# Kernel optimization log

Measured on AMD Instinct MI355X. Metric: run time of the kernel, lower is better.

Reference implementation:

```python
import jax, jax.numpy as jnp
import numpy as np

B, T, N, D = 128, 5, 64, 4
F1, F2 = 32, 32            # cnn filters
H = 128                    # mlp hidden units
PRED_STEPS = 8

# fully-connected adjacency without self-loops (fc_matrix)
_adj = np.ones((N, N)) - np.eye(N)
SRC, TGT = np.where(_adj)
SRC = jnp.asarray(SRC)
TGT = jnp.asarray(TGT)
E = int(SRC.shape[0])      # N*(N-1) = 4032


def _glorot(key, shape):
    fan_in = shape[-2] if len(shape) >= 2 else shape[0]
    return jax.random.normal(key, shape, jnp.float32) * float(1.0 / np.sqrt(fan_in))


def setup_inputs() -> dict:
    key = jax.random.key(0)
    ks = jax.random.split(key, 16)
    inp = {
        'time_segs': jax.random.normal(ks[0], (B, T, N, D), jnp.float32),
        # Conv1D over time: two valid convs, kernel 3
        'cw1': _glorot(ks[1], (3, D, F1)), 'cb1': jnp.zeros((F1,), jnp.float32),
        'cw2': _glorot(ks[2], (3, F1, F2)), 'cb2': jnp.zeros((F2,), jnp.float32),
        # edge encoder MLP: 2*F2 -> H -> H
        'ew1': _glorot(ks[3], (2 * F2, H)), 'eb1': jnp.zeros((H,), jnp.float32),
        'ew2': _glorot(ks[4], (H, H)), 'eb2': jnp.zeros((H,), jnp.float32),
        # node encoder MLP: H -> H -> H
        'nw1': _glorot(ks[5], (H, H)), 'nb1': jnp.zeros((H,), jnp.float32),
        'nw2': _glorot(ks[6], (H, H)), 'nb2': jnp.zeros((H,), jnp.float32),
        # node decoder MLP: (D + H) -> H -> H
        'dw1': _glorot(ks[7], (D + H, H)), 'db1': jnp.zeros((H,), jnp.float32),
        'dw2': _glorot(ks[8], (H, H)), 'db2': jnp.zeros((H,), jnp.float32),
        # output dense: H -> D
        'ow': _glorot(ks[9], (H, D)), 'ob': jnp.zeros((D,), jnp.float32),
    }
    return inp


def _mlp(x, w1, b1, w2, b2):
    h = jax.nn.relu(x @ w1 + b1)
    return jax.nn.relu(h @ w2 + b2)


def _conv_time(x, w, b):
    # x: [B, N, t, C]; valid conv (kernel 3) over time axis, relu
    b_, n_, t_, c_ = x.shape
    y = jax.lax.conv_general_dilated(
        x.reshape(b_ * n_, t_, c_), w, window_strides=(1,), padding='VALID',
        dimension_numbers=('NWC', 'WIO', 'NWC'))
    y = jax.nn.relu(y + b)
    return y.reshape(b_, n_, y.shape[1], y.shape[2])


def reference(time_segs, cw1, cb1, cw2, cb2, ew1, eb1, ew2, eb2,
              nw1, nb1, nw2, nb2, dw1, db1, dw2, db2, ow, ob):
    # [B, T, N, D] -> [B, N, T, D]
    window = jnp.transpose(time_segs, (0, 2, 1, 3))
    preds = []
    for _ in range(PRED_STEPS):
        # condense time: [B, N, 5, D] -> [B, N, 1, F2]
        h = _conv_time(window, cw1, cb1)
        h = _conv_time(h, cw2, cb2)
        # gather source/target node states per edge -> [B, E, 1, 2*F2]
        edge_in = jnp.concatenate([h[:, SRC], h[:, TGT]], axis=-1)
        edge_msg = _mlp(edge_in, ew1, eb1, ew2, eb2)           # [B, E, 1, H]
        # scatter-sum edge messages to target nodes -> [B, N, 1, H]
        node_msg = jnp.zeros((window.shape[0], N, 1, edge_msg.shape[-1]),
                             edge_msg.dtype).at[:, TGT].add(edge_msg)
        node_msg = _mlp(node_msg, nw1, nb1, nw2, nb2)
        prev = window[:, :, -1:, :]                            # [B, N, 1, D]
        dec = _mlp(jnp.concatenate([prev, node_msg], axis=-1), dw1, db1, dw2, db2)
        nxt = dec @ ow + ob + prev                             # residual, [B, N, 1, D]
        preds.append(nxt)
        window = jnp.concatenate([window[:, :, 1:, :], nxt], axis=2)
    out = jnp.concatenate(preds, axis=2)                       # [B, N, P, D]
    return jnp.transpose(out, (0, 2, 1, 3))                    # [B, P, N, D]
```

## Files before the change

kernel.cpp:

```cpp
#include <hip/hip_runtime.h>

#define WROW 52
#define TG 8

typedef _Float16 half_t;
typedef _Float16 half8 __attribute__((ext_vector_type(8)));
typedef float f32x4 __attribute__((ext_vector_type(4)));

#define SC 0.0009765625f

__device__ __forceinline__ unsigned pkrtz(float a, float b) {
  auto v = __builtin_amdgcn_cvt_pkrtz(a, b);
  return *(unsigned*)&v;
}

template<int LANES>
__device__ __forceinline__ void conv_proj(
    int lane, int gid, float* cp,
    const float* __restrict__ cw1, const float* __restrict__ cb1,
    const float* __restrict__ cw2, const float* __restrict__ cb2,
    const float* __restrict__ ew1,
    float* __restrict__ an, float* __restrict__ bn)
{
  #pragma unroll
  for (int o = 0; o < 96 / LANES; ++o) {
    int idx = lane + o * LANES;
    int tt = idx >> 5, f = idx & 31;
    float a = cb1[f];
    #pragma unroll
    for (int kt = 0; kt < 3; ++kt)
      #pragma unroll
      for (int d = 0; d < 4; ++d)
        a = fmaf(cp[(tt + kt) * 4 + d], cw1[(kt * 4 + d) * 32 + f], a);
    cp[32 + idx] = fmaxf(a, 0.f);
  }
  __syncthreads();
  #pragma unroll
  for (int o = 0; o < 32 / LANES; ++o) {
    int f = lane + o * LANES;
    float a = cb2[f];
    #pragma unroll
    for (int kt = 0; kt < 3; ++kt)
      for (int f1 = 0; f1 < 32; ++f1)
        a = fmaf(cp[32 + kt * 32 + f1], cw2[(kt * 32 + f1) * 32 + f], a);
    cp[128 + f] = fmaxf(a, 0.f);
  }
  __syncthreads();
  #pragma unroll
  for (int o = 0; o < 128 / LANES; ++o) {
    int j = lane + o * LANES;
    float a = 0.f, bb = 0.f;
    for (int f = 0; f < 32; ++f) {
      float h = cp[128 + f];
      a  = fmaf(h, ew1[f * 128 + j], a);
      bb = fmaf(h, ew1[(32 + f) * 128 + j], bb);
    }
    an[gid * 128 + j] = a * SC;
    bn[gid * 128 + j] = bb * SC;
  }
}

__global__ __launch_bounds__(256) void k_init(
    const float* __restrict__ ts,
    const float* __restrict__ cw1, const float* __restrict__ cb1,
    const float* __restrict__ cw2, const float* __restrict__ cb2,
    const float* __restrict__ ew1,
    float* __restrict__ win, float* __restrict__ an, float* __restrict__ bn)
{
  __shared__ float cp[16 * 160];
  int blk = blockIdx.x;
  int b = blk >> 2, n0 = (blk & 3) << 4;
  int tid = threadIdx.x;
  int ln = tid >> 4, lane = tid & 15;
  int n = n0 + ln;
  int gid = b * 64 + n;
  float* mycp = cp + ln * 160;
  for (int idx = lane; idx < 20; idx += 16) {
    int tt = idx >> 2, d = idx & 3;
    float v = ts[((b * 5 + tt) * 64 + n) * 4 + d];
    mycp[idx] = v;
    win[gid * WROW + idx] = v;
  }
  __syncthreads();
  conv_proj<16>(lane, gid, mycp, cw1, cb1, cw2, cb2, ew1, an, bn);
}

__global__ __launch_bounds__(256) void k_wsplit(
    const float* __restrict__ ew2, const float* __restrict__ nw1,
    const float* __restrict__ nw2, const float* __restrict__ dw1,
    const float* __restrict__ dw2, half_t* __restrict__ dst)
{
  int mat = blockIdx.x >> 6;
  const float* src = (mat == 0) ? ew2 : (mat == 1) ? nw1 : (mat == 2) ? nw2
                   : (mat == 3) ? (dw1 + 512) : dw2;
  half_t* dh = dst + mat * 2 * 16384;
  half_t* dl = dh + 16384;
  int g = (blockIdx.x & 63) * 256 + threadIdx.x;
  int k = g >> 7, col = g & 127;
  float x = src[g];
  _Float16 hi = (_Float16)x;
  float lo = x - (float)hi;
  int c = col >> 4, kb = k >> 5, kk = k & 31;
  int lane = ((kk >> 3) << 4) | (col & 15);
  int j = kk & 7;
  int idx = ((c * 4 + kb) * 64 + lane) * 8 + j;
  dh[idx] = hi;
  dl[idx] = (_Float16)lo;
}

__global__ __launch_bounds__(256, 2) void k_edge_v8(
    const float* __restrict__ an, const float* __restrict__ bn,
    const float* __restrict__ eb1, const float* __restrict__ eb2,
    const half_t* __restrict__ Bh, const half_t* __restrict__ Bl,
    float* __restrict__ nm)
{
  __shared__ __align__(16) half_t sAh[8192];
  __shared__ __align__(16) half_t sAl[8192];
  __shared__ float s_bt[TG * 128];
  int blk = blockIdx.x;
  int b = blk & 127, t0 = (blk >> 7) * TG;
  int tid = threadIdx.x;
  int w = tid >> 6, lane = tid & 63;

  #pragma unroll
  for (int i = 0; i < TG * 128 / 256; ++i) {
    int idx = tid + (i << 8);
    int tt = idx >> 7, j = idx & 127;
    s_bt[idx] = bn[((b << 6) + t0 + tt) * 128 + j] + eb1[j] * SC;
  }

  float au[4][8];
  {
    int kb8 = tid >> 4, sl = tid & 15;
    #pragma unroll
    for (int it = 0; it < 4; ++it) {
      const float* ap = an + (b << 13) + ((it * 16 + sl) << 7) + (kb8 << 3);
      float4 x0 = *(const float4*)ap;
      float4 x1 = *(const float4*)(ap + 4);
      au[it][0] = x0.x; au[it][1] = x0.y; au[it][2] = x0.z; au[it][3] = x0.w;
      au[it][4] = x1.x; au[it][5] = x1.y; au[it][6] = x1.z; au[it][7] = x1.w;
    }
  }

  half8 rbh[2][4], rbl[2][4];
  #pragma unroll
  for (int cc = 0; cc < 2; ++cc)
    #pragma unroll
    for (int kb = 0; kb < 4; ++kb) {
      int c = w * 2 + cc;
      rbh[cc][kb] = *(const half8*)(Bh + ((c * 4 + kb) * 64 + lane) * 8);
      rbl[cc][kb] = *(const half8*)(Bl + ((c * 4 + kb) * 64 + lane) * 8);
    }

  float bias0 = eb2[(w * 2 + 0) * 16 + (lane & 15)];
  float bias1 = eb2[(w * 2 + 1) * 16 + (lane & 15)];
  int rowoff = (lane >> 4) * 4;

  __syncthreads();

  for (int tt = 0; tt < TG; ++tt) {
    {
      const float* bp = s_bt + (tt << 7) + ((tid >> 4) << 3);
      float4 b0 = *(const float4*)bp;
      float4 b1 = *(const float4*)(bp + 4);
      float bs[8] = {b0.x, b0.y, b0.z, b0.w, b1.x, b1.y, b1.z, b1.w};
      #pragma unroll
      for (int it = 0; it < 4; ++it) {
        int u = tid + (it << 8);
        float h32[8], l32[8];
        #pragma unroll
        for (int i = 0; i < 8; ++i) {
          float x = fmaxf(au[it][i] + bs[i], 0.f);
          float h = __uint_as_float(__float_as_uint(x) & 0xffffe000u);
          h32[i] = h;
          l32[i] = x - h;
        }
        unsigned hw[4], lw[4];
        #pragma unroll
        for (int p = 0; p < 4; ++p) {
          hw[p] = pkrtz(h32[2 * p], h32[2 * p + 1]);
          lw[p] = pkrtz(l32[2 * p], l32[2 * p + 1]);
        }
        *(uint4*)(sAh + u * 8) = make_uint4(hw[0], hw[1], hw[2], hw[3]);
        *(uint4*)(sAl + u * 8) = make_uint4(lw[0], lw[1], lw[2], lw[3]);
      }
    }
    __syncthreads();

    f32x4 acc[4][2];
    #pragma unroll
    for (int rr = 0; rr < 4; ++rr)
      #pragma unroll
      for (int cc = 0; cc < 2; ++cc)
        acc[rr][cc] = (f32x4){0.f, 0.f, 0.f, 0.f};

    #pragma unroll
    for (int kb = 0; kb < 4; ++kb) {
      half8 ah[4], al[4];
      #pragma unroll
      for (int rr = 0; rr < 4; ++rr) {
        ah[rr] = *(const half8*)(sAh + ((rr * 4 + kb) * 64 + lane) * 8);
        al[rr] = *(const half8*)(sAl + ((rr * 4 + kb) * 64 + lane) * 8);
      }
      #pragma unroll
      for (int cc = 0; cc < 2; ++cc)
        #pragma unroll
        for (int rr = 0; rr < 4; ++rr) {
          acc[rr][cc] = __builtin_amdgcn_mfma_f32_16x16x32_f16(ah[rr], rbh[cc][kb], acc[rr][cc], 0, 0, 0);
          acc[rr][cc] = __builtin_amdgcn_mfma_f32_16x16x32_f16(ah[rr], rbl[cc][kb], acc[rr][cc], 0, 0, 0);
          acc[rr][cc] = __builtin_amdgcn_mfma_f32_16x16x32_f16(al[rr], rbh[cc][kb], acc[rr][cc], 0, 0, 0);
        }
    }

    int t = t0 + tt;
    float csum0 = 0.f, csum1 = 0.f;
    #pragma unroll
    for (int rr = 0; rr < 4; ++rr) {
      int sbase = rr * 16 + rowoff;
      #pragma unroll
      for (int q = 0; q < 4; ++q) {
        int s = sbase + q;
        float y0 = acc[rr][0][q] * 1024.f + bias0;
        float y1 = acc[rr][1][q] * 1024.f + bias1;
        if (s != t) {
          csum0 += fmaxf(y0, 0.f);
          csum1 += fmaxf(y1, 0.f);
        }
      }
    }
    csum0 += __shfl_xor(csum0, 16, 64);
    csum0 += __shfl_xor(csum0, 32, 64);
    csum1 += __shfl_xor(csum1, 16, 64);
    csum1 += __shfl_xor(csum1, 32, 64);
    if (lane < 32)
      nm[((b << 6) + t) * 128 + w * 32 + lane] = (lane < 16) ? csum0 : csum1;
    __syncthreads();
  }
}

__global__ __launch_bounds__(256) void k_nd_mfma(
    int step,
    const float* __restrict__ nm,
    const half_t* __restrict__ wsp,
    const float* __restrict__ nb1, const float* __restrict__ nb2,
    const float* __restrict__ dw1, const float* __restrict__ db1,
    const float* __restrict__ db2,
    const float* __restrict__ ow,  const float* __restrict__ ob,
    const float* __restrict__ cw1, const float* __restrict__ cb1,
    const float* __restrict__ cw2, const float* __restrict__ cb2,
    const float* __restrict__ ew1,
    float* __restrict__ win, float* __restrict__ an, float* __restrict__ bn,
    float* __restrict__ out)
{
  __shared__ __align__(16) float Xraw[16][132];
  __shared__ __align__(16) half_t sAh[2048];
  __shared__ __align__(16) half_t sAl[2048];
  __shared__ float sP[16][4];
  __shared__ float s_dw1a[4 * 128];
  __shared__ float s_nxt[16][4];
  __shared__ float cp[16 * 160];

  int blk = blockIdx.x;
  int b = blk >> 2, n0 = (blk & 3) << 4;
  int tid = threadIdx.x;
  int w = tid >> 6, lane = tid & 63;

  #pragma unroll
  for (int i = 0; i < 2; ++i) {
    int idx = tid + (i << 8);
    int row = idx >> 5, jf = idx & 31;
    *(float4*)&Xraw[row][jf << 2] =
        *(const float4*)(nm + ((b * 64 + n0 + row) << 7) + (jf << 2));
  }
  if (tid < 64) {
    int ln = tid >> 2, d = tid & 3;
    sP[ln][d] = win[(b * 64 + n0 + ln) * WROW + (step + 4) * 4 + d];
  }
  for (int idx = tid; idx < 512; idx += 256) s_dw1a[idx] = dw1[idx];
  __syncthreads();

  auto splitX = [&]() {
    int kb = tid >> 6, l = tid & 63;
    int row = l & 15, k0 = (kb << 5) + ((l >> 4) << 3);
    float h32[8], l32[8];
    #pragma unroll
    for (int i = 0; i < 8; ++i) {
      float x = Xraw[row][k0 + i] * SC;
      float h = __uint_as_float(__float_as_uint(x) & 0xffffe000u);
      h32[i] = h;
      l32[i] = x - h;
    }
    unsigned hw[4], lw[4];
    #pragma unroll
    for (int p = 0; p < 4; ++p) {
      hw[p] = pkrtz(h32[2 * p], h32[2 * p + 1]);
      lw[p] = pkrtz(l32[2 * p], l32[2 * p + 1]);
    }
    *(uint4*)(sAh + tid * 8) = make_uint4(hw[0], hw[1], hw[2], hw[3]);
    *(uint4*)(sAl + tid * 8) = make_uint4(lw[0], lw[1], lw[2], lw[3]);
  };

  auto layerM = [&](const half_t* Wh, const half_t* Wl,
                    const float* bias, bool withP) {
    splitX();
    __syncthreads();
    #pragma unroll
    for (int cc = 0; cc < 2; ++cc) {
      int c = w * 2 + cc;
      int col = c * 16 + (lane & 15);
      int row0 = (lane >> 4) * 4;
      float bj = bias[col];
      f32x4 acc;
      #pragma unroll
      for (int q = 0; q < 4; ++q) {
        float v = bj;
        if (withP) {
          #pragma unroll
          for (int d = 0; d < 4; ++d)
            v = fmaf(sP[row0 + q][d], s_dw1a[d * 128 + col], v);
        }
        acc[q] = v * SC;
      }
      #pragma unroll
      for (int kb = 0; kb < 4; ++kb) {
        half8 ah = *(const half8*)(sAh + ((kb << 6) + lane) * 8);
        half8 al = *(const half8*)(sAl + ((kb << 6) + lane) * 8);
        half8 bh = *(const half8*)(Wh + ((c * 4 + kb) * 64 + lane) * 8);
        half8 bl = *(const half8*)(Wl + ((c * 4 + kb) * 64 + lane) * 8);
        acc = __builtin_amdgcn_mfma_f32_16x16x32_f16(ah, bh, acc, 0, 0, 0);
        acc = __builtin_amdgcn_mfma_f32_16x16x32_f16(ah, bl, acc, 0, 0, 0);
        acc = __builtin_amdgcn_mfma_f32_16x16x32_f16(al, bh, acc, 0, 0, 0);
      }
      #pragma unroll
      for (int q = 0; q < 4; ++q)
        Xraw[row0 + q][col] = fmaxf(acc[q] * 1024.f, 0.f);
    }
    __syncthreads();
  };

  const half_t* nh1 = wsp + 2 * 16384;  const half_t* nl1 = nh1 + 16384;
  const half_t* nh2 = wsp + 4 * 16384;  const half_t* nl2 = nh2 + 16384;
  const half_t* dh1 = wsp + 6 * 16384;  const half_t* dl1 = dh1 + 16384;
  const half_t* dh2 = wsp + 8 * 16384;  const half_t* dl2 = dh2 + 16384;

  layerM(nh1, nl1, nb1, false);
  layerM(nh2, nl2, nb2, false);
  layerM(dh1, dl1, db1, true);
  layerM(dh2, dl2, db2, false);

  {
    int ln = tid >> 4, d = (tid >> 2) & 3, kq = tid & 3;
    float cs = 0.f;
    #pragma unroll
    for (int i = 0; i < 32; ++i) {
      int k = (kq << 5) + i;
      cs = fmaf(Xraw[ln][k], ow[k * 4 + d], cs);
    }
    cs += __shfl_xor(cs, 1, 64);
    cs += __shfl_xor(cs, 2, 64);
    if ((tid & 3) == 0) {
      float a = cs + ob[d] + sP[ln][d];
      int n = n0 + ln, gid = b * 64 + n;
      win[gid * WROW + (step + 5) * 4 + d] = a;
      out[((b * 8 + step) * 64 + n) * 4 + d] = a;
      s_nxt[ln][d] = a;
    }
  }
  __syncthreads();

  if (step < 7) {
    int ln = tid >> 4, lane2 = tid & 15;
    int gid = b * 64 + n0 + ln;
    float* mycp = cp + ln * 160;
    mycp[lane2] = win[gid * WROW + (step + 1) * 4 + lane2];
    if (lane2 < 4) mycp[16 + lane2] = s_nxt[ln][lane2];
    __syncthreads();
    conv_proj<16>(lane2, gid, mycp, cw1, cb1, cw2, cb2, ew1, an, bn);
  }
}

extern "C" void kernel_launch(void* const* d_in, const int* in_sizes, int n_in,
                              void* d_out, int out_size, void* d_ws, size_t ws_size,
                              hipStream_t stream) {
  (void)in_sizes; (void)n_in; (void)out_size; (void)ws_size;
  const float* ts  = (const float*)d_in[0];
  const float* cw1 = (const float*)d_in[1];
  const float* cb1 = (const float*)d_in[2];
  const float* cw2 = (const float*)d_in[3];
  const float* cb2 = (const float*)d_in[4];
  const float* ew1 = (const float*)d_in[5];
  const float* eb1 = (const float*)d_in[6];
  const float* ew2 = (const float*)d_in[7];
  const float* eb2 = (const float*)d_in[8];
  const float* nw1 = (const float*)d_in[9];
  const float* nb1 = (const float*)d_in[10];
  const float* nw2 = (const float*)d_in[11];
  const float* nb2 = (const float*)d_in[12];
  const float* dw1 = (const float*)d_in[13];
  const float* db1 = (const float*)d_in[14];
  const float* dw2 = (const float*)d_in[15];
  const float* db2 = (const float*)d_in[16];
  const float* ow  = (const float*)d_in[17];
  const float* ob  = (const float*)d_in[18];
  float* out = (float*)d_out;
  float* ws  = (float*)d_ws;
  float* win = ws;
  float* an  = win + 425984;
  float* bn  = an + 1048576;
  float* nmb = bn + 1048576;
  half_t* wsp = (half_t*)(nmb + 1048576);
  half_t* Bh = wsp;
  half_t* Bl = Bh + 16384;

  hipLaunchKernelGGL(k_wsplit, dim3(320), dim3(256), 0, stream,
                     ew2, nw1, nw2, dw1, dw2, wsp);
  hipLaunchKernelGGL(k_init, dim3(512), dim3(256), 0, stream,
                     ts, cw1, cb1, cw2, cb2, ew1, win, an, bn);
  for (int k = 0; k < 8; ++k) {
    hipLaunchKernelGGL(k_edge_v8, dim3(1024), dim3(256), 0, stream,
                       an, bn, eb1, eb2, Bh, Bl, nmb);
    hipLaunchKernelGGL(k_nd_mfma, dim3(512), dim3(256), 0, stream,
                       k, nmb, wsp, nb1, nb2, dw1, db1, db2,
                       ow, ob, cw1, cb1, cw2, cb2, ew1, win, an, bn, out);
  }
}
```

Before: 610.4 us.

## Fuse edge and node/decoder kernels into one per-step kernel with ping-pong buffers

Merges the edge-message kernel and the node/decoder kernel into a single kernel per prediction step. Each block now handles 16 target nodes (TG raised to 16), keeps the summed node messages in shared memory, and runs the node and decoder MLPs and the next-step conv projection directly. This removes the global round-trip of the node-message buffer and halves the number of launches. The an/bn projections are double-buffered because blocks now write the next step's projections while other blocks may still be reading the current ones. The cost is fewer, heavier blocks (512 instead of 1024) and a shared-memory union that has to stay alias-safe.

After: 531.2 us. -13.0%, faster.

```diff
diff --git a/kernel.cpp b/kernel.cpp
--- a/kernel.cpp
+++ b/kernel.cpp
@@ -1,7 +1,7 @@
 #include <hip/hip_runtime.h>
 
 #define WROW 52
-#define TG 8
+#define TG 16
 
 typedef _Float16 half_t;
 typedef _Float16 half8 __attribute__((ext_vector_type(8)));
@@ -108,25 +108,46 @@
   dl[idx] = (_Float16)lo;
 }
 
-__global__ __launch_bounds__(256, 2) void k_edge_v8(
-    const float* __restrict__ an, const float* __restrict__ bn,
+__global__ __launch_bounds__(256, 2) void k_step(
+    int step,
+    const float* __restrict__ anR, const float* __restrict__ bnR,
+    float* __restrict__ anW, float* __restrict__ bnW,
     const float* __restrict__ eb1, const float* __restrict__ eb2,
-    const half_t* __restrict__ Bh, const half_t* __restrict__ Bl,
-    float* __restrict__ nm)
+    const half_t* __restrict__ wsp,
+    const float* __restrict__ nb1, const float* __restrict__ nb2,
+    const float* __restrict__ dw1, const float* __restrict__ db1,
+    const float* __restrict__ db2,
+    const float* __restrict__ ow,  const float* __restrict__ ob,
+    const float* __restrict__ cw1, const float* __restrict__ cb1,
+    const float* __restrict__ cw2, const float* __restrict__ cb2,
+    const float* __restrict__ ew1,
+    float* __restrict__ win, float* __restrict__ out)
 {
-  __shared__ __align__(16) half_t sAh[8192];
-  __shared__ __align__(16) half_t sAl[8192];
-  __shared__ float s_bt[TG * 128];
+  __shared__ __align__(16) unsigned char smem[40960];
+  __shared__ __align__(16) float X[16][132];
+  half_t* sAh = (half_t*)smem;
+  half_t* sAl = (half_t*)(smem + 16384);
+  float*  s_bt = (float*)(smem + 32768);
+  half_t* nAh = (half_t*)smem;
+  half_t* nAl = (half_t*)(smem + 4096);
+  float*  cp     = (float*)(smem + 16640);
+  float*  s_dw1a = (float*)(smem + 26880);
+  float (*sP)[4]   = (float(*)[4])(smem + 28928);
+  float (*s_nxt)[4] = (float(*)[4])(smem + 29184);
+
   int blk = blockIdx.x;
   int b = blk & 127, t0 = (blk >> 7) * TG;
   int tid = threadIdx.x;
   int w = tid >> 6, lane = tid & 63;
 
+  const half_t* Bh = wsp;
+  const half_t* Bl = wsp + 16384;
+
   #pragma unroll
   for (int i = 0; i < TG * 128 / 256; ++i) {
     int idx = tid + (i << 8);
     int tt = idx >> 7, j = idx & 127;
-    s_bt[idx] = bn[((b << 6) + t0 + tt) * 128 + j] + eb1[j] * SC;
+    s_bt[idx] = bnR[((b << 6) + t0 + tt) * 128 + j] + eb1[j] * SC;
   }
 
   float au[4][8];
@@ -134,7 +155,7 @@
     int kb8 = tid >> 4, sl = tid & 15;
     #pragma unroll
     for (int it = 0; it < 4; ++it) {
-      const float* ap = an + (b << 13) + ((it * 16 + sl) << 7) + (kb8 << 3);
+      const float* ap = anR + (b << 13) + ((it * 16 + sl) << 7) + (kb8 << 3);
       float4 x0 = *(const float4*)ap;
       float4 x1 = *(const float4*)(ap + 4);
       au[it][0] = x0.x; au[it][1] = x0.y; au[it][2] = x0.z; au[it][3] = x0.w;
@@ -233,48 +254,13 @@
     csum1 += __shfl_xor(csum1, 16, 64);
     csum1 += __shfl_xor(csum1, 32, 64);
     if (lane < 32)
-      nm[((b << 6) + t) * 128 + w * 32 + lane] = (lane < 16) ? csum0 : csum1;
+      X[tt][w * 32 + lane] = (lane < 16) ? csum0 : csum1;
     __syncthreads();
   }
-}
-
-__global__ __launch_bounds__(256) void k_nd_mfma(
-    int step,
-    const float* __restrict__ nm,
-    const half_t* __restrict__ wsp,
-    const float* __restrict__ nb1, const float* __restrict__ nb2,
-    const float* __restrict__ dw1, const float* __restrict__ db1,
-    const float* __restrict__ db2,
-    const float* __restrict__ ow,  const float* __restrict__ ob,
-    const float* __restrict__ cw1, const float* __restrict__ cb1,
-    const float* __restrict__ cw2, const float* __restrict__ cb2,
-    const float* __restrict__ ew1,
-    float* __restrict__ win, float* __restrict__ an, float* __restrict__ bn,
-    float* __restrict__ out)
-{
-  __shared__ __align__(16) float Xraw[16][132];
-  __shared__ __align__(16) half_t sAh[2048];
-  __shared__ __align__(16) half_t sAl[2048];
-  __shared__ float sP[16][4];
-  __shared__ float s_dw1a[4 * 128];
-  __shared__ float s_nxt[16][4];
-  __shared__ float cp[16 * 160];
-
-  int blk = blockIdx.x;
-  int b = blk >> 2, n0 = (blk & 3) << 4;
-  int tid = threadIdx.x;
-  int w = tid >> 6, lane = tid & 63;
-
-  #pragma unroll
-  for (int i = 0; i < 2; ++i) {
-    int idx = tid + (i << 8);
-    int row = idx >> 5, jf = idx & 31;
-    *(float4*)&Xraw[row][jf << 2] =
-        *(const float4*)(nm + ((b * 64 + n0 + row) << 7) + (jf << 2));
-  }
+
   if (tid < 64) {
     int ln = tid >> 2, d = tid & 3;
-    sP[ln][d] = win[(b * 64 + n0 + ln) * WROW + (step + 4) * 4 + d];
+    sP[ln][d] = win[(b * 64 + t0 + ln) * WROW + (step + 4) * 4 + d];
   }
   for (int idx = tid; idx < 512; idx += 256) s_dw1a[idx] = dw1[idx];
   __syncthreads();
@@ -285,7 +271,7 @@
     float h32[8], l32[8];
     #pragma unroll
     for (int i = 0; i < 8; ++i) {
-      float x = Xraw[row][k0 + i] * SC;
+      float x = X[row][k0 + i] * SC;
       float h = __uint_as_float(__float_as_uint(x) & 0xffffe000u);
       h32[i] = h;
       l32[i] = x - h;
@@ -296,8 +282,8 @@
       hw[p] = pkrtz(h32[2 * p], h32[2 * p + 1]);
       lw[p] = pkrtz(l32[2 * p], l32[2 * p + 1]);
     }
-    *(uint4*)(sAh + tid * 8) = make_uint4(hw[0], hw[1], hw[2], hw[3]);
-    *(uint4*)(sAl + tid * 8) = make_uint4(lw[0], lw[1], lw[2], lw[3]);
+    *(uint4*)(nAh + tid * 8) = make_uint4(hw[0], hw[1], hw[2], hw[3]);
+    *(uint4*)(nAl + tid * 8) = make_uint4(lw[0], lw[1], lw[2], lw[3]);
   };
 
   auto layerM = [&](const half_t* Wh, const half_t* Wl,
@@ -323,8 +309,8 @@
       }
       #pragma unroll
       for (int kb = 0; kb < 4; ++kb) {
-        half8 ah = *(const half8*)(sAh + ((kb << 6) + lane) * 8);
-        half8 al = *(const half8*)(sAl + ((kb << 6) + lane) * 8);
+        half8 ah = *(const half8*)(nAh + ((kb << 6) + lane) * 8);
+        half8 al = *(const half8*)(nAl + ((kb << 6) + lane) * 8);
         half8 bh = *(const half8*)(Wh + ((c * 4 + kb) * 64 + lane) * 8);
         half8 bl = *(const half8*)(Wl + ((c * 4 + kb) * 64 + lane) * 8);
         acc = __builtin_amdgcn_mfma_f32_16x16x32_f16(ah, bh, acc, 0, 0, 0);
@@ -333,7 +319,7 @@
       }
       #pragma unroll
       for (int q = 0; q < 4; ++q)
-        Xraw[row0 + q][col] = fmaxf(acc[q] * 1024.f, 0.f);
+        X[row0 + q][col] = fmaxf(acc[q] * 1024.f, 0.f);
     }
     __syncthreads();
   };
@@ -354,13 +340,13 @@
     #pragma unroll
     for (int i = 0; i < 32; ++i) {
       int k = (kq << 5) + i;
-      cs = fmaf(Xraw[ln][k], ow[k * 4 + d], cs);
+      cs = fmaf(X[ln][k], ow[k * 4 + d], cs);
     }
     cs += __shfl_xor(cs, 1, 64);
     cs += __shfl_xor(cs, 2, 64);
     if ((tid & 3) == 0) {
       float a = cs + ob[d] + sP[ln][d];
-      int n = n0 + ln, gid = b * 64 + n;
+      int n = t0 + ln, gid = b * 64 + n;
       win[gid * WROW + (step + 5) * 4 + d] = a;
       out[((b * 8 + step) * 64 + n) * 4 + d] = a;
       s_nxt[ln][d] = a;
@@ -370,12 +356,12 @@
 
   if (step < 7) {
     int ln = tid >> 4, lane2 = tid & 15;
-    int gid = b * 64 + n0 + ln;
+    int gid = b * 64 + t0 + ln;
     float* mycp = cp + ln * 160;
     mycp[lane2] = win[gid * WROW + (step + 1) * 4 + lane2];
     if (lane2 < 4) mycp[16 + lane2] = s_nxt[ln][lane2];
     __syncthreads();
-    conv_proj<16>(lane2, gid, mycp, cw1, cb1, cw2, cb2, ew1, an, bn);
+    conv_proj<16>(lane2, gid, mycp, cw1, cb1, cw2, cb2, ew1, anW, bnW);
   }
 }
 
@@ -405,22 +391,24 @@
   float* out = (float*)d_out;
   float* ws  = (float*)d_ws;
   float* win = ws;
-  float* an  = win + 425984;
-  float* bn  = an + 1048576;
-  float* nmb = bn + 1048576;
-  half_t* wsp = (half_t*)(nmb + 1048576);
-  half_t* Bh = wsp;
-  half_t* Bl = Bh + 16384;
+  float* an0 = win + 425984;
+  float* bn0 = an0 + 1048576;
+  float* an1 = bn0 + 1048576;
+  float* bn1 = an1 + 1048576;
+  half_t* wsp = (half_t*)(bn1 + 1048576);
 
   hipLaunchKernelGGL(k_wsplit, dim3(320), dim3(256), 0, stream,
                      ew2, nw1, nw2, dw1, dw2, wsp);
   hipLaunchKernelGGL(k_init, dim3(512), dim3(256), 0, stream,
-                     ts, cw1, cb1, cw2, cb2, ew1, win, an, bn);
+                     ts, cw1, cb1, cw2, cb2, ew1, win, an0, bn0);
   for (int k = 0; k < 8; ++k) {
-    hipLaunchKernelGGL(k_edge_v8, dim3(1024), dim3(256), 0, stream,
-                       an, bn, eb1, eb2, Bh, Bl, nmb);
-    hipLaunchKernelGGL(k_nd_mfma, dim3(512), dim3(256), 0, stream,
-                       k, nmb, wsp, nb1, nb2, dw1, db1, db2,
-                       ow, ob, cw1, cb1, cw2, cb2, ew1, win, an, bn, out);
-  }
-}
+    const float* anR = (k & 1) ? an1 : an0;
+    const float* bnR = (k & 1) ? bn1 : bn0;
+    float* anW = (k & 1) ? an0 : an1;
+    float* bnW = (k & 1) ? bn0 : bn1;
+    hipLaunchKernelGGL(k_step, dim3(512), dim3(256), 0, stream,
+                       k, anR, bnR, anW, bnW, eb1, eb2, wsp,
+                       nb1, nb2, dw1, db1, db2, ow, ob,
+                       cw1, cb1, cw2, cb2, ew1, win, out);
+  }
+}
```
